# Kernel optimization log

Measured on AMD Instinct MI355X. Metric: run time of the kernel, lower is better.

Reference implementation:

```python
import math
import jax, jax.numpy as jnp
import numpy as np

B, L, D = 2, 2048, 1024
H, KV, HD = 16, 4, 64
G = H // KV  # heads per kv group
SCALE = 1.0 / math.sqrt(HD)
NUM_SEGMENTS = 4


def alibi_slopes(num_heads):
    # power-of-two branch of _compute_alibi_slopes
    base = 2.0 ** (-(2.0 ** (-(math.log2(num_heads) - 3))))
    return jnp.asarray([base ** i for i in range(1, num_heads + 1)], dtype=jnp.float32)


def setup_inputs() -> dict:
    key = jax.random.key(0)
    k0, k1, k2, k3, k4, k5 = jax.random.split(key, 6)
    s = 0.02
    hidden_states = jax.random.normal(k0, (B, L, D), dtype=jnp.float32)
    segment_ids = jnp.sort(jax.random.randint(k1, (B, L), 0, NUM_SEGMENTS), axis=-1).astype(jnp.int32)
    Wq = jax.random.normal(k2, (D, H * HD), dtype=jnp.float32) * s
    Wk = jax.random.normal(k3, (D, KV * HD), dtype=jnp.float32) * s
    Wv = jax.random.normal(k4, (D, KV * HD), dtype=jnp.float32) * s
    Wo = jax.random.normal(k5, (H * HD, D), dtype=jnp.float32) * s
    return {"hidden_states": hidden_states, "segment_ids": segment_ids,
            "Wq": Wq, "Wk": Wk, "Wv": Wv, "Wo": Wo}


def reference(hidden_states, segment_ids, Wq, Wk, Wv, Wo):
    b, l, _ = hidden_states.shape
    # projections
    q = (hidden_states @ Wq).reshape(b, l, H, HD).transpose(0, 2, 1, 3)      # [B,H,L,hd]
    k = (hidden_states @ Wk).reshape(b, l, KV, HD).transpose(0, 2, 1, 3)     # [B,KV,L,hd]
    v = (hidden_states @ Wv).reshape(b, l, KV, HD).transpose(0, 2, 1, 3)     # [B,KV,L,hd]
    # GQA grouping: head h -> kv head h // G (kernel semantics)
    qg = q.reshape(b, KV, G, l, HD)                                          # [B,KV,G,L,hd]
    scores = jnp.einsum('bgpqd,bgkd->bgpqk', qg, k) * SCALE                  # [B,KV,G,Lq,Lk]
    # ALiBi: bias = -slope_h * |i - j|
    slopes = alibi_slopes(H).reshape(KV, G)                                   # head h = kv*G + p
    pos = jnp.arange(l, dtype=jnp.float32)
    dist = jnp.abs(pos[:, None] - pos[None, :])                               # [L,L]
    scores = scores - slopes[None, :, :, None, None] * dist[None, None, None, :, :]
    # causal + segment mask
    causal = pos[:, None] >= pos[None, :]                                     # [L,L]
    same_seg = (segment_ids[:, :, None] == segment_ids[:, None, :]) & (segment_ids[:, :, None] >= 0)  # [B,L,L]
    valid = same_seg[:, None, None, :, :] & causal[None, None, None, :, :]
    scores = jnp.where(valid, scores, -jnp.inf)
    attn = jax.nn.softmax(scores, axis=-1)
    out = jnp.einsum('bgpqk,bgkd->bgpqd', attn, v)                            # [B,KV,G,L,hd]
    out = out.reshape(b, H, l, HD).transpose(0, 2, 1, 3).reshape(b, l, H * HD)
    return out @ Wo
```

## Files before the change

### kernel.cpp

```cpp
#include <hip/hip_runtime.h>
#include <hip/hip_bf16.h>
#include <type_traits>

#define DI __device__ __forceinline__

typedef unsigned short u16;
typedef unsigned int u32;
typedef __bf16 bf16x8 __attribute__((ext_vector_type(8)));
typedef u16 u16x8 __attribute__((ext_vector_type(8)));
typedef float f32x4 __attribute__((ext_vector_type(4)));
typedef float f32x16 __attribute__((ext_vector_type(16)));
typedef u32 u32x2 __attribute__((ext_vector_type(2)));
typedef u32 u32x4 __attribute__((ext_vector_type(4)));

constexpr int Bb = 2, Ls = 2048, Hh = 16, KVh = 4, HD = 64;
constexpr float LOG2E = 1.44269504088896f;
constexpr float RSQ2 = 0.70710678118654752f;

DI u16 f2bf(float f) {
  __hip_bfloat16 h = __float2bfloat16(f);
  return __builtin_bit_cast(u16, h);
}

DI u32 cvtpk(float lo, float hi) {
  u32 r;
  asm("v_cvt_pk_bf16_f32 %0, %1, %2" : "=v"(r) : "v"(lo), "v"(hi));
  return r;
}

DI void pls(u32& a, u32& b) {
  asm("v_permlane32_swap_b32 %0, %1" : "+v"(a), "+v"(b));
}
DI float sum_halves(float v) {
  u32 a = __builtin_bit_cast(u32, v), b = a;
  pls(a, b);
  return __builtin_bit_cast(float, a) + __builtin_bit_cast(float, b);
}
DI float max_halves(float v) {
  u32 a = __builtin_bit_cast(u32, v), b = a;
  pls(a, b);
  return fmaxf(__builtin_bit_cast(float, a), __builtin_bit_cast(float, b));
}

DI f32x4 mfma16(bf16x8 a, bf16x8 b, f32x4 c) {
  return __builtin_amdgcn_mfma_f32_16x16x32_bf16(a, b, c, 0, 0, 0);
}
DI f32x16 mfma32(bf16x8 a, bf16x8 b, f32x16 c) {
  return __builtin_amdgcn_mfma_f32_32x32x16_bf16(a, b, c, 0, 0, 0);
}
DI bf16x8 bc(u32x4 v) { return __builtin_bit_cast(bf16x8, v); }

DI void gld16(const u16* g, u16* l) {
  __builtin_amdgcn_global_load_lds(
      (const __attribute__((address_space(1))) u32*)g,
      (__attribute__((address_space(3))) u32*)l, 16, 0, 0);
}

__global__ void prep(const float* __restrict__ hs, u16* __restrict__ hsb,
                     const int* __restrict__ seg, int* __restrict__ sst,
                     const float* __restrict__ Wq, const float* __restrict__ Wk,
                     const float* __restrict__ Wv, const float* __restrict__ Wo,
                     u16* __restrict__ wqkvT, u16* __restrict__ woT) {
  int bid = blockIdx.x;
  if (bid < 4096) {
    int i = bid * 256 + threadIdx.x;
    float4 v = reinterpret_cast<const float4*>(hs)[i];
    ushort4 o;
    o.x = f2bf(v.x); o.y = f2bf(v.y); o.z = f2bf(v.z); o.w = f2bf(v.w);
    reinterpret_cast<ushort4*>(hsb)[i] = o;
    return;
  }
  if (bid < 4112) {
    int idx = bid - 4096;
    int b = idx >> 3;
    int l = (idx & 7) * 256 + threadIdx.x;
    const int* s = seg + b * Ls;
    int v = s[l];
    int lo = 0, hi = l;
    while (lo < hi) {
      int mid = (lo + hi) >> 1;
      if (s[mid] < v) lo = mid + 1; else hi = mid;
    }
    sst[b * Ls + l] = lo;
    return;
  }
  int t = bid - 4112;
  const float* in; u16* out; int N, rowoff, x, y;
  if (t < 1024)      { in = Wq; out = wqkvT; N = 1024; rowoff = 0;
                       x = t & 31; y = t >> 5; }
  else if (t < 1280) { in = Wk; out = wqkvT; N = 256; rowoff = 1024;
                       int u = t - 1024; x = u & 7; y = u >> 3; }
  else if (t < 1536) { in = Wv; out = wqkvT; N = 256; rowoff = 1280;
                       int u = t - 1280; x = u & 7; y = u >> 3; }
  else               { in = Wo; out = woT; N = 1024; rowoff = 0;
                       int u = t - 1536; x = u & 31; y = u >> 5; }
  __shared__ u16 tl[32][33];
  int k0 = y * 32, n0 = x * 32;
  int tx = threadIdx.x & 31, ty = threadIdx.x >> 5;
#pragma unroll
  for (int i = ty; i < 32; i += 8)
    tl[i][tx] = f2bf(in[(size_t)(k0 + i) * N + n0 + tx]);
  __syncthreads();
#pragma unroll
  for (int i = ty; i < 32; i += 8)
    out[(size_t)(rowoff + n0 + i) * 1024 + k0 + tx] = tl[tx][i];
}

template <int MODE>
__global__ __launch_bounds__(512) void gemm_bt(
    const u16* __restrict__ A, const u16* __restrict__ Bt,
    float* __restrict__ C, u16* __restrict__ Qf, u16* __restrict__ Kf,
    u16* __restrict__ Vf, int M, int N, int K) {
  __shared__ u16 lA[4][128 * 32];
  __shared__ u16 lB[4][128 * 32];
  const int m0 = blockIdx.y * 128, n0 = blockIdx.x * 128;
  const int tid = threadIdx.x;
  const int lane = tid & 63;
  const int wr = ((tid >> 8) & 1) * 64;
  const int wc = ((tid >> 6) & 3) * 32;
  const int lr = lane & 15, lk = (lane >> 4) * 8;
  const int r0 = tid >> 2, c0 = (tid & 3) * 8;
  const int woff = (tid & 0x1C0) << 4;
  const u16* pA0 = &A[(size_t)(m0 + r0) * K + c0];
  const u16* pB0 = &Bt[(size_t)(n0 + r0) * K + c0];

  auto stage = [&](u16* sA, u16* sB, int k0) {
    gld16(pA0 + k0, (u16*)((char*)sA + woff));
    gld16(pB0 + k0, (u16*)((char*)sB + woff));
  };

  f32x4 acc[4][2] = {};
  auto compute = [&](const u16* sA, const u16* sB) {
    bf16x8 af[4], bfv[2];
#pragma unroll
    for (int m = 0; m < 4; m++)
      af[m] = *reinterpret_cast<const bf16x8*>(&sA[(wr + m * 16 + lr) * 32 + lk]);
#pragma unroll
    for (int n = 0; n < 2; n++)
      bfv[n] = *reinterpret_cast<const bf16x8*>(&sB[(wc + n * 16 + lr) * 32 + lk]);
#pragma unroll
    for (int m = 0; m < 4; m++)
#pragma unroll
      for (int n = 0; n < 2; n++)
        acc[m][n] = mfma16(af[m], bfv[n], acc[m][n]);
  };

#define BODY(B, VM, KC, DOST)                                        \
  do {                                                               \
    asm volatile("s_waitcnt vmcnt(" VM ")" ::: "memory");            \
    __builtin_amdgcn_s_barrier();                                    \
    asm volatile("" ::: "memory");                                   \
    if (DOST) stage(lA[(B + 3) & 3], lB[(B + 3) & 3], (KC) + 96);    \
    compute(lA[B], lB[B]);                                           \
  } while (0)

  stage(lA[0], lB[0], 0);
  stage(lA[1], lB[1], 32);
  stage(lA[2], lB[2], 64);
  int k0 = 0;
  for (; k0 + 224 <= K; k0 += 128) {
    BODY(0, "4", k0, 1);
    BODY(1, "4", k0 + 32, 1);
    BODY(2, "4", k0 + 64, 1);
    BODY(3, "4", k0 + 96, 1);
  }
  BODY(0, "4", k0, 1);
  BODY(1, "4", k0 + 32, 0);
  BODY(2, "2", k0 + 64, 0);
  BODY(3, "0", k0 + 96, 0);
#undef BODY

  const int rr = (lane >> 4) * 4, cc = lane & 15;
#pragma unroll
  for (int m = 0; m < 4; m++) {
    int row0 = m0 + wr + m * 16 + rr;
#pragma unroll
    for (int n = 0; n < 2; n++) {
      int col = n0 + wc + n * 16 + cc;
      if constexpr (MODE == 0) {
#pragma unroll
        for (int r = 0; r < 4; r++)
          C[(size_t)(row0 + r) * N + col] = acc[m][n][r];
      } else {
        int bb = row0 >> 11, l = row0 & 2047;
        int d = col & 63, c8 = d >> 3, d7 = d & 7;
        int kt = l >> 5, r32 = l & 31;
        if (col < 1024) {
          int hd = col >> 6;
          u16* base = &Qf[((((size_t)(bb * 16 + hd) * 64 + kt) << 11)) +
                          ((c8 * 32 + r32) << 3) + d7];
#pragma unroll
          for (int r = 0; r < 4; r++) base[r * 8] = f2bf(acc[m][n][r]);
        } else if (col < 1280) {
          int kv = (col - 1024) >> 6;
          u16* base = &Kf[((((size_t)(bb * 4 + kv) * 64 + kt) << 11)) +
                          ((c8 * 32 + r32) << 3) + d7];
#pragma unroll
          for (int r = 0; r < 4; r++) base[r * 8] = f2bf(acc[m][n][r]);
        } else {
          int kv = (col - 1280) >> 6;
          ushort4 pv;
          pv.x = f2bf(acc[m][n][0]); pv.y = f2bf(acc[m][n][1]);
          pv.z = f2bf(acc[m][n][2]); pv.w = f2bf(acc[m][n][3]);
          *reinterpret_cast<ushort4*>(
              &Vf[((((size_t)(bb * 4 + kv) * 64 + kt) << 11)) +
                  ((((l >> 3) & 3) * 64 + d) << 3) + (l & 7)]) = pv;
        }
      }
    }
  }
}

__global__ __launch_bounds__(64, 1) void attn(
    const u16* __restrict__ Qf, const u16* __restrict__ Kf,
    const u16* __restrict__ Vf, const int* __restrict__ sst,
    u16* __restrict__ Obuf) {
  const int qt = 63 - blockIdx.x;
  const int hp = blockIdx.y, b = blockIdx.z;
  const int h0 = hp << 1;
  const int kvh = h0 >> 2;
  const int lane = threadIdx.x;
  const int qi = lane & 31, hi = lane >> 5;
  const int qw = qt * 32;
  const int q = qw + qi;
  const float slope0 = __builtin_amdgcn_exp2f(-0.5f * (float)(h0 + 1));
  const float SL0 = slope0 * LOG2E;
  const float SL1 = SL0 * RSQ2;
  const float SL0x32 = 32.f * SL0, SL1x32 = 32.f * SL1;
  const float Cs = 0.125f * LOG2E;
  const u16* Qt0 = Qf + (((size_t)(b * Hh + h0) * 64 + qt) << 11);
  const u16* Qt1 = Qt0 + ((size_t)64 << 11);
  const u16* Kbase = Kf + (((size_t)(b * KVh + kvh) * 64) << 11);
  const u16* Vbase = Vf + (((size_t)(b * KVh + kvh) * 64) << 11);

  bf16x8 qfA[4], qfB[4];
#pragma unroll
  for (int c = 0; c < 4; c++) {
    qfA[c] = *reinterpret_cast<const bf16x8*>(&Qt0[((2 * c + hi) * 32 + qi) * 8]);
    qfB[c] = *reinterpret_cast<const bf16x8*>(&Qt1[((2 * c + hi) * 32 + qi) * 8]);
  }

  const int start = sst[b * Ls + q];
  const int smax = __shfl(start, 31);
  const int k_begin = __shfl(start, 0) & ~31;

  float krsl[16];
#pragma unroll
  for (int r = 0; r < 16; r++)
    krsl[r] = (float)((r & 3) + 8 * (r >> 2) + 4 * hi) * SL0;
  float biasA = (float)(k_begin - q) * SL0;
  float biasB = (float)(k_begin - q) * SL1;
  float lA = 0.f, lB = 0.f;
  f32x16 oAlo = {}, oAhi = {}, oBlo = {}, oBhi = {};

  auto KLD = [&](int kt, u32x4* dst) {
    const u16* p = Kbase + ((size_t)kt << 11);
#pragma unroll
    for (int c = 0; c < 4; c++)
      dst[c] = *reinterpret_cast<const u32x4*>(&p[((2 * c + hi) * 32 + qi) * 8]);
  };
  auto VLD = [&](int kt, u32x4* dst) {
    const u16* p = Vbase + ((size_t)kt << 11);
#pragma unroll
    for (int j = 0; j < 4; j++) {
      int off = ((((j & 1) * 2 + hi) * 64) + (j >> 1) * 32 + qi) * 8;
      dst[j] = *reinterpret_cast<const u32x4*>(&p[off]);
    }
  };

  auto rowmax = [&](const float* t) {
    float u0 = fmaxf(t[0], t[1]), u1 = fmaxf(t[2], t[3]);
    float u2 = fmaxf(t[4], t[5]), u3 = fmaxf(t[6], t[7]);
    float u4 = fmaxf(t[8], t[9]), u5 = fmaxf(t[10], t[11]);
    float u6 = fmaxf(t[12], t[13]), u7 = fmaxf(t[14], t[15]);
    u0 = fmaxf(u0, u1); u2 = fmaxf(u2, u3);
    u4 = fmaxf(u4, u5); u6 = fmaxf(u6, u7);
    return fmaxf(fmaxf(u0, u2), fmaxf(u4, u6));
  };

  auto body = [&](int kk, u32x4* KR, u32x4* VR) {
    f32x16 aA = {}, aB = {};
    __builtin_amdgcn_s_setprio(1);
#pragma unroll
    for (int c = 0; c < 4; c++) aA = mfma32(bc(KR[c]), qfA[c], aA);
#pragma unroll
    for (int c = 0; c < 4; c++) aB = mfma32(bc(KR[c]), qfB[c], aB);
    __builtin_amdgcn_s_setprio(0);
    const int kt2 = min(kk + 64, qw) >> 5;
    KLD(kt2, KR);

    float tA[16], tB[16];
#pragma unroll
    for (int r = 0; r < 16; r++) {
      tA[r] = fmaf(aA[r], Cs, biasA) + krsl[r];
      tB[r] = fmaf(aB[r], Cs, biasB) + krsl[r] * RSQ2;
    }
    if (!(kk >= smax && kk < qw)) {
#pragma unroll
      for (int r = 0; r < 16; r++) {
        int j = kk + (r & 3) + 8 * (r >> 2) + 4 * hi;
        bool v = (j >= start) && (j <= q);
        tA[r] = v ? tA[r] : -3.0e38f;
        tB[r] = v ? tB[r] : -3.0e38f;
      }
    }
    {
      float mt = max_halves(rowmax(tA));
      if (!__all(mt <= 8.f)) {
        float dm = fmaxf(mt, 0.f);
        float fac = __builtin_amdgcn_exp2f(-dm);
        biasA -= dm; lA *= fac;
#pragma unroll
        for (int r = 0; r < 16; r++) { oAlo[r] *= fac; oAhi[r] *= fac; tA[r] -= dm; }
      }
    }
    {
      float mt = max_halves(rowmax(tB));
      if (!__all(mt <= 8.f)) {
        float dm = fmaxf(mt, 0.f);
        float fac = __builtin_amdgcn_exp2f(-dm);
        biasB -= dm; lB *= fac;
#pragma unroll
        for (int r = 0; r < 16; r++) { oBlo[r] *= fac; oBhi[r] *= fac; tB[r] -= dm; }
      }
    }
    float pA[16], pB[16];
#pragma unroll
    for (int r = 0; r < 16; r++) {
      pA[r] = __builtin_amdgcn_exp2f(tA[r]);
      pB[r] = __builtin_amdgcn_exp2f(tB[r]);
    }
    float tsA = 0.f, tsB = 0.f;
#pragma unroll
    for (int r = 0; r < 16; r++) { tsA += pA[r]; tsB += pB[r]; }
    lA += sum_halves(tsA);
    lB += sum_halves(tsB);

    u32 pkA[8], pkB[8];
#pragma unroll
    for (int i = 0; i < 8; i++) {
      pkA[i] = cvtpk(pA[2 * i], pA[2 * i + 1]);
      pkB[i] = cvtpk(pB[2 * i], pB[2 * i + 1]);
    }
    pls(pkA[0], pkA[2]); pls(pkA[1], pkA[3]);
    pls(pkA[4], pkA[6]); pls(pkA[5], pkA[7]);
    pls(pkB[0], pkB[2]); pls(pkB[1], pkB[3]);
    pls(pkB[4], pkB[6]); pls(pkB[5], pkB[7]);
    u32x4 fA0 = { pkA[0], pkA[1], pkA[2], pkA[3] };
    u32x4 fA1 = { pkA[4], pkA[5], pkA[6], pkA[7] };
    u32x4 fB0 = { pkB[0], pkB[1], pkB[2], pkB[3] };
    u32x4 fB1 = { pkB[4], pkB[5], pkB[6], pkB[7] };

    __builtin_amdgcn_s_setprio(1);
    oAlo = mfma32(bc(VR[0]), bc(fA0), oAlo);
    oAlo = mfma32(bc(VR[1]), bc(fA1), oAlo);
    oAhi = mfma32(bc(VR[2]), bc(fA0), oAhi);
    oAhi = mfma32(bc(VR[3]), bc(fA1), oAhi);
    oBlo = mfma32(bc(VR[0]), bc(fB0), oBlo);
    oBlo = mfma32(bc(VR[1]), bc(fB1), oBlo);
    oBhi = mfma32(bc(VR[2]), bc(fB0), oBhi);
    oBhi = mfma32(bc(VR[3]), bc(fB1), oBhi);
    __builtin_amdgcn_s_setprio(0);
    VLD(kt2, VR);
    biasA += SL0x32; biasB += SL1x32;
  };

  u32x4 KR0[4], VR0[4], KR1[4], VR1[4];
  {
    const int kt0 = k_begin >> 5;
    const int kt1 = min(k_begin + 32, qw) >> 5;
    KLD(kt0, KR0); VLD(kt0, VR0);
    KLD(kt1, KR1); VLD(kt1, VR1);
  }
  int kk = k_begin;
  while (true) {
    body(kk, KR0, VR0);
    if (kk + 32 > qw) break;
    body(kk + 32, KR1, VR1);
    if (kk + 64 > qw) break;
    kk += 64;
  }

  const float invA = __builtin_amdgcn_rcpf(lA);
  const float invB = __builtin_amdgcn_rcpf(lB);
  const size_t orow = (size_t)(b * Ls + q) * 1024 + h0 * 64;
#pragma unroll
  for (int g = 0; g < 4; g++) {
    int d0 = g * 8 + hi * 4;
    u32x2 pa = { cvtpk(oAlo[4 * g + 0] * invA, oAlo[4 * g + 1] * invA),
                 cvtpk(oAlo[4 * g + 2] * invA, oAlo[4 * g + 3] * invA) };
    u32x2 pb = { cvtpk(oAhi[4 * g + 0] * invA, oAhi[4 * g + 1] * invA),
                 cvtpk(oAhi[4 * g + 2] * invA, oAhi[4 * g + 3] * invA) };
    *reinterpret_cast<u32x2*>(&Obuf[orow + d0]) = pa;
    *reinterpret_cast<u32x2*>(&Obuf[orow + 32 + d0]) = pb;
    u32x2 qa = { cvtpk(oBlo[4 * g + 0] * invB, oBlo[4 * g + 1] * invB),
                 cvtpk(oBlo[4 * g + 2] * invB, oBlo[4 * g + 3] * invB) };
    u32x2 qb = { cvtpk(oBhi[4 * g + 0] * invB, oBhi[4 * g + 1] * invB),
                 cvtpk(oBhi[4 * g + 2] * invB, oBhi[4 * g + 3] * invB) };
    *reinterpret_cast<u32x2*>(&Obuf[orow + 64 + d0]) = qa;
    *reinterpret_cast<u32x2*>(&Obuf[orow + 96 + d0]) = qb;
  }
}

extern "C" void kernel_launch(void* const* d_in, const int* in_sizes, int n_in,
                              void* d_out, int out_size, void* d_ws, size_t ws_size,
                              hipStream_t stream) {
  const float* hs = (const float*)d_in[0];
  const int* seg = (const int*)d_in[1];
  const float* Wq = (const float*)d_in[2];
  const float* Wk = (const float*)d_in[3];
  const float* Wv = (const float*)d_in[4];
  const float* Wo = (const float*)d_in[5];
  float* out = (float*)d_out;
  char* ws = (char*)d_ws;
  u16* hsb   = (u16*)(ws);
  u16* wqkvT = (u16*)(ws + 8388608);
  u16* woT   = (u16*)(ws + 11534336);
  u16* qf    = (u16*)(ws + 13631488);
  u16* kf    = (u16*)(ws + 22020096);
  u16* vf    = (u16*)(ws + 24117248);
  int* sst   = (int*)(ws + 26214400);
  u16* obuf  = hsb;

  prep<<<dim3(6672), dim3(256), 0, stream>>>(hs, hsb, seg, sst,
                                             Wq, Wk, Wv, Wo, wqkvT, woT);
  gemm_bt<1><<<dim3(12, 32), dim3(512), 0, stream>>>(
      hsb, wqkvT, nullptr, qf, kf, vf, 4096, 1536, 1024);
  attn<<<dim3(64, 8, 2), dim3(64), 0, stream>>>(qf, kf, vf, sst, obuf);
  gemm_bt<0><<<dim3(8, 32), dim3(512), 0, stream>>>(
      obuf, woT, out, nullptr, nullptr, nullptr, 4096, 1024, 1024);
}
```

Baseline: 80.15 us.

## Split attention KV loop across two waves and XOR-swizzle GEMM LDS

The attention kernel now runs two wavefronts per block. Each wave processes alternating 32-key tiles with its own online-softmax state, and the partial results are merged through shared memory by rescaling with the accumulated max offsets. The goal is twice the parallelism on the long causal KV loop. The cost is a shared-memory merge, a barrier, and losing the double-buffered prefetch of the next tile. Separately, the GEMM applies an XOR swizzle to the LDS column offsets for both the stage writes and the fragment reads, aiming to reduce LDS bank conflicts.

```diff
diff --git a/kernel.cpp b/kernel.cpp
--- a/kernel.cpp
+++ b/kernel.cpp
@@ -118,8 +118,10 @@
   const int lane = tid & 63;
   const int wr = ((tid >> 8) & 1) * 64;
   const int wc = ((tid >> 6) & 3) * 32;
-  const int lr = lane & 15, lk = (lane >> 4) * 8;
-  const int r0 = tid >> 2, c0 = (tid & 3) * 8;
+  const int lr = lane & 15;
+  const int lk = (((lane >> 4) ^ (lane & 3)) * 8);
+  const int r0 = tid >> 2;
+  const int c0 = (((tid & 3) ^ ((tid >> 2) & 3)) * 8);
   const int woff = (tid & 0x1C0) << 4;
   const u16* pA0 = &A[(size_t)(m0 + r0) * K + c0];
   const u16* pB0 = &Bt[(size_t)(n0 + r0) * K + c0];
@@ -211,7 +213,7 @@
   }
 }
 
-__global__ __launch_bounds__(64, 1) void attn(
+__global__ __launch_bounds__(128, 1) void attn(
     const u16* __restrict__ Qf, const u16* __restrict__ Kf,
     const u16* __restrict__ Vf, const int* __restrict__ sst,
     u16* __restrict__ Obuf) {
@@ -219,14 +221,15 @@
   const int hp = blockIdx.y, b = blockIdx.z;
   const int h0 = hp << 1;
   const int kvh = h0 >> 2;
-  const int lane = threadIdx.x;
+  const int tid = threadIdx.x;
+  const int w = tid >> 6, lane = tid & 63;
   const int qi = lane & 31, hi = lane >> 5;
   const int qw = qt * 32;
   const int q = qw + qi;
   const float slope0 = __builtin_amdgcn_exp2f(-0.5f * (float)(h0 + 1));
   const float SL0 = slope0 * LOG2E;
   const float SL1 = SL0 * RSQ2;
-  const float SL0x32 = 32.f * SL0, SL1x32 = 32.f * SL1;
+  const float SL0x64 = 64.f * SL0, SL1x64 = 64.f * SL1;
   const float Cs = 0.125f * LOG2E;
   const u16* Qt0 = Qf + (((size_t)(b * Hh + h0) * 64 + qt) << 11);
   const u16* Qt1 = Qt0 + ((size_t)64 << 11);
@@ -248,8 +251,9 @@
 #pragma unroll
   for (int r = 0; r < 16; r++)
     krsl[r] = (float)((r & 3) + 8 * (r >> 2) + 4 * hi) * SL0;
-  float biasA = (float)(k_begin - q) * SL0;
-  float biasB = (float)(k_begin - q) * SL1;
+  float biasA = (float)(k_begin + 32 * w - q) * SL0;
+  float biasB = (float)(k_begin + 32 * w - q) * SL1;
+  float mAacc = 0.f, mBacc = 0.f;
   float lA = 0.f, lB = 0.f;
   f32x16 oAlo = {}, oAhi = {}, oBlo = {}, oBhi = {};
 
@@ -309,7 +313,7 @@
       if (!__all(mt <= 8.f)) {
         float dm = fmaxf(mt, 0.f);
         float fac = __builtin_amdgcn_exp2f(-dm);
-        biasA -= dm; lA *= fac;
+        biasA -= dm; lA *= fac; mAacc += dm;
 #pragma unroll
         for (int r = 0; r < 16; r++) { oAlo[r] *= fac; oAhi[r] *= fac; tA[r] -= dm; }
       }
@@ -319,7 +323,7 @@
       if (!__all(mt <= 8.f)) {
         float dm = fmaxf(mt, 0.f);
         float fac = __builtin_amdgcn_exp2f(-dm);
-        biasB -= dm; lB *= fac;
+        biasB -= dm; lB *= fac; mBacc += dm;
 #pragma unroll
         for (int r = 0; r < 16; r++) { oBlo[r] *= fac; oBhi[r] *= fac; tB[r] -= dm; }
       }
@@ -362,23 +366,42 @@
     oBhi = mfma32(bc(VR[3]), bc(fB1), oBhi);
     __builtin_amdgcn_s_setprio(0);
     VLD(kt2, VR);
-    biasA += SL0x32; biasB += SL1x32;
-  };
-
-  u32x4 KR0[4], VR0[4], KR1[4], VR1[4];
+    biasA += SL0x64; biasB += SL1x64;
+  };
+
+  u32x4 KR[4], VR[4];
+  int kk = k_begin + 32 * w;
+  if (kk <= qw) { KLD(kk >> 5, KR); VLD(kk >> 5, VR); }
+  for (; kk <= qw; kk += 64) body(kk, KR, VR);
+
+  __shared__ float sm[64][69];
+  if (w == 1) {
+#pragma unroll
+    for (int r = 0; r < 16; r++) {
+      sm[lane][r] = oAlo[r];      sm[lane][16 + r] = oAhi[r];
+      sm[lane][32 + r] = oBlo[r]; sm[lane][48 + r] = oBhi[r];
+    }
+    sm[lane][64] = lA; sm[lane][65] = lB;
+    sm[lane][66] = mAacc; sm[lane][67] = mBacc;
+  }
+  __syncthreads();
+  if (w == 1) return;
   {
-    const int kt0 = k_begin >> 5;
-    const int kt1 = min(k_begin + 32, qw) >> 5;
-    KLD(kt0, KR0); VLD(kt0, VR0);
-    KLD(kt1, KR1); VLD(kt1, VR1);
-  }
-  int kk = k_begin;
-  while (true) {
-    body(kk, KR0, VR0);
-    if (kk + 32 > qw) break;
-    body(kk + 32, KR1, VR1);
-    if (kk + 64 > qw) break;
-    kk += 64;
+    float mA1 = sm[lane][66], mB1 = sm[lane][67];
+    float MA = fmaxf(mAacc, mA1), MB = fmaxf(mBacc, mB1);
+    float fa0 = __builtin_amdgcn_exp2f(mAacc - MA);
+    float fa1 = __builtin_amdgcn_exp2f(mA1 - MA);
+    float fb0 = __builtin_amdgcn_exp2f(mBacc - MB);
+    float fb1 = __builtin_amdgcn_exp2f(mB1 - MB);
+    lA = lA * fa0 + sm[lane][64] * fa1;
+    lB = lB * fb0 + sm[lane][65] * fb1;
+#pragma unroll
+    for (int r = 0; r < 16; r++) {
+      oAlo[r] = oAlo[r] * fa0 + sm[lane][r] * fa1;
+      oAhi[r] = oAhi[r] * fa0 + sm[lane][16 + r] * fa1;
+      oBlo[r] = oBlo[r] * fb0 + sm[lane][32 + r] * fb1;
+      oBhi[r] = oBhi[r] * fb0 + sm[lane][48 + r] * fb1;
+    }
   }
 
   const float invA = __builtin_amdgcn_rcpf(lA);
@@ -426,7 +449,7 @@
                                              Wq, Wk, Wv, Wo, wqkvT, woT);
   gemm_bt<1><<<dim3(12, 32), dim3(512), 0, stream>>>(
       hsb, wqkvT, nullptr, qf, kf, vf, 4096, 1536, 1024);
-  attn<<<dim3(64, 8, 2), dim3(64), 0, stream>>>(qf, kf, vf, sst, obuf);
+  attn<<<dim3(64, 8, 2), dim3(128), 0, stream>>>(qf, kf, vf, sst, obuf);
   gemm_bt<0><<<dim3(8, 32), dim3(512), 0, stream>>>(
       obuf, woT, out, nullptr, nullptr, nullptr, 4096, 1024, 1024);
 }
```

After: 78.91 us. No clear change (-1.5%).
